# Kernel optimization log

Hardware: AMD Instinct MI355X
Metric: run time of the kernel (lower is better)

## Reference

```python
import jax, jax.numpy as jnp
import numpy as np

B, H, S, D = 4, 16, 2048, 64
SCALE = 8.0  # sqrt(D)
NEG = -1000000000.0


def setup_inputs() -> dict:
    key = jax.random.key(0)
    kq, kk, kv = jax.random.split(key, 3)
    q = jax.random.normal(kq, (B, H, S, D), dtype=jnp.float32)
    k = jax.random.normal(kk, (B, H, S, D), dtype=jnp.float32)
    v = jax.random.normal(kv, (B, H, S, D), dtype=jnp.float32)
    # causal mask: True means masked out (matches torch masked_fill)
    mask = jnp.triu(jnp.ones((S, S), dtype=bool), k=1)[None, None, :, :]
    mask = jnp.broadcast_to(mask, (B, 1, S, S))
    return {"q": q, "k": k, "v": v, "mask": mask}


def reference(q, k, v, mask):
    # score = q @ k^T / scale  -> [B,H,S,S]
    score = jnp.einsum("bhqd,bhkd->bhqk", q, k) / SCALE
    score = jnp.where(mask, NEG, score)
    probs = jax.nn.softmax(score, axis=-1)
    context = jnp.einsum("bhqk,bhkd->bhqd", probs, v)
    return context
```

## Files before the change

kernel.cpp:

```cpp
#include <hip/hip_runtime.h>

#define SQ 2048
#define DH 64
#define BK 64
#define NQT 32
#define NBH 64
#define M0 8.0f

#define WS_BYTES ((size_t)2 * NBH * SQ * DH * 2)

typedef float f32x4 __attribute__((ext_vector_type(4)));
typedef __bf16 bf16x8 __attribute__((ext_vector_type(8)));
typedef _Float16 f16x4 __attribute__((ext_vector_type(4)));
typedef __fp16 fp16x2 __attribute__((ext_vector_type(2)));
typedef unsigned short u16x8 __attribute__((ext_vector_type(8)));
typedef unsigned int u32x4 __attribute__((ext_vector_type(4)));

static __device__ __forceinline__ unsigned int pkbf(float a, float b) {
#if __has_builtin(__builtin_amdgcn_cvt_pk_bf16_f32)
  typedef __bf16 bf16x2 __attribute__((ext_vector_type(2)));
  bf16x2 r = __builtin_amdgcn_cvt_pk_bf16_f32(a, b);
  return __builtin_bit_cast(unsigned int, r);
#else
  unsigned int ua = __builtin_bit_cast(unsigned int, a);
  unsigned int ub = __builtin_bit_cast(unsigned int, b);
  ua += 0x7fffu + ((ua >> 16) & 1u);
  ub += 0x7fffu + ((ub >> 16) & 1u);
  return (ua >> 16) | (ub & 0xffff0000u);
#endif
}

static __device__ __forceinline__ unsigned int pkf16(float a, float b) {
  fp16x2 r = __builtin_amdgcn_cvt_pkrtz(a, b);
  return __builtin_bit_cast(unsigned int, r);
}

static __device__ __forceinline__ f32x4 mfma_qk(u16x8 a, u16x8 b, f32x4 c) {
  return __builtin_amdgcn_mfma_f32_16x16x32_bf16(
      __builtin_bit_cast(bf16x8, a), __builtin_bit_cast(bf16x8, b), c, 0, 0, 0);
}

static __device__ __forceinline__ f32x4 mfma_pv(f16x4 a, f16x4 b, f32x4 c) {
  return __builtin_amdgcn_mfma_f32_16x16x16f16(a, b, c, 0, 0, 0);
}

static __device__ __forceinline__ void ld16(unsigned short* l, const unsigned short* g) {
  __builtin_amdgcn_global_load_lds(
      (const __attribute__((address_space(1))) unsigned int*)(const void*)g,
      (__attribute__((address_space(3))) unsigned int*)(void*)l, 16, 0, 0);
}

static __device__ __forceinline__ void store_tile(float* wb, float* dst,
                                                  const f32x4* o, int lane,
                                                  int l15, int quad) {
#pragma unroll
  for (int dt = 0; dt < 4; ++dt) {
    const int colw = dt * 16 + quad * 4;
    *(f32x4*)&wb[l15 * 64 + (colw ^ ((l15 & 3) * 16))] = o[dt];
  }
  __builtin_amdgcn_wave_barrier();
#pragma unroll
  for (int j = 0; j < 4; ++j) {
    const int row = j * 4 + (lane >> 4);
    const int colw = (lane & 15) * 4;
    f32x4 v = *(const f32x4*)&wb[row * 64 + (colw ^ ((row & 3) * 16))];
    *(f32x4*)&dst[row * 64 + colw] = v;
  }
}

__global__ __launch_bounds__(256) void prep(const float* __restrict__ K,
                                            const float* __restrict__ V,
                                            unsigned short* __restrict__ Kb,
                                            unsigned short* __restrict__ Vt) {
  const int bh = (int)blockIdx.x >> 5;
  const int st = (int)blockIdx.x & 31;
  const int tid = threadIdx.x;
  __shared__ __align__(16) unsigned short T[DH * 64];
  {
    const int r = tid >> 2, c0 = (tid & 3) * 16;
    const float* kp = K + ((size_t)bh * SQ + st * 64 + r) * DH + c0;
    f32x4 x0 = *(const f32x4*)kp, x1 = *(const f32x4*)(kp + 4),
          x2 = *(const f32x4*)(kp + 8), x3 = *(const f32x4*)(kp + 12);
    u32x4 w0 = {pkbf(x0[0], x0[1]), pkbf(x0[2], x0[3]), pkbf(x1[0], x1[1]), pkbf(x1[2], x1[3])};
    u32x4 w1 = {pkbf(x2[0], x2[1]), pkbf(x2[2], x2[3]), pkbf(x3[0], x3[1]), pkbf(x3[2], x3[3])};
    unsigned short* kb = Kb + ((size_t)bh * SQ + st * 64 + r) * DH + c0;
    *(u32x4*)kb = w0;
    *(u32x4*)(kb + 8) = w1;
  }
  {
    const int kvb = (tid >> 4) * 4, vdb = (tid & 15) * 4;
    const float* vp = V + ((size_t)bh * SQ + st * 64 + kvb) * DH + vdb;
    f32x4 r0 = *(const f32x4*)vp, r1 = *(const f32x4*)(vp + DH),
          r2 = *(const f32x4*)(vp + 2 * DH), r3 = *(const f32x4*)(vp + 3 * DH);
    const int uu = kvb >> 3, h = (kvb >> 2) & 1;
#pragma unroll
    for (int i = 0; i < 4; ++i) {
      const int d = vdb + i;
      uint2 w = {pkf16(r0[i], r1[i]), pkf16(r2[i], r3[i])};
      *(uint2*)&T[d * 64 + ((uu ^ (d & 7)) * 8) + h * 4] = w;
    }
  }
  __syncthreads();
  {
    const int d2 = tid >> 2, cp = (tid & 3) * 2;
#pragma unroll
    for (int e = 0; e < 2; ++e) {
      const int uu = cp + e;
      u16x8 val = *(const u16x8*)&T[d2 * 64 + ((uu ^ (d2 & 7)) * 8)];
      *(u16x8*)&Vt[(size_t)bh * DH * SQ + (size_t)d2 * SQ + st * 64 + uu * 8] = val;
    }
  }
}

__global__ __launch_bounds__(256, 4) void fa_main(
    const float* __restrict__ Q, const unsigned short* __restrict__ Kb,
    const unsigned short* __restrict__ Vt, float* __restrict__ O) {
  const int lin = (int)blockIdx.x;
  const int xcd = lin & 7, u = lin >> 3, hh = u & 7, p = u >> 3;
  const int bh = hh * 8 + xcd;
  const int qtl = p, qth = NQT - 1 - p;

  const int tid = threadIdx.x;
  const int wv = tid >> 6;
  const int lane = tid & 63;
  const int l15 = lane & 15;
  const int quad = lane >> 4;

  __shared__ __align__(16) unsigned short S0[2 * BK * DH];
  __shared__ __align__(16) unsigned short S1[2 * BK * DH];

  const size_t hq = (size_t)bh * (SQ * DH);
  const unsigned short* KbH = Kb + (size_t)bh * SQ * DH;
  const unsigned short* VtH = Vt + (size_t)bh * DH * SQ;

  const int srow = wv * 16 + (lane >> 3);
  const int sc = lane & 7;

  u16x8 qfl[2], qfh[2];
  {
    const float scq = 0.125f * 1.4426950408889634f;
#pragma unroll
    for (int g = 0; g < 2; ++g) {
      const int wq0 = (g ? qth : qtl) * 64 + wv * 16;
      const float* qp = Q + hq + (size_t)(wq0 + l15) * DH + quad * 8;
#pragma unroll
      for (int c = 0; c < 2; ++c) {
        f32x4 x = *(const f32x4*)(qp + c * 32);
        f32x4 y = *(const f32x4*)(qp + c * 32 + 4);
        u32x4 w = {pkbf(x[0] * scq, x[1] * scq), pkbf(x[2] * scq, x[3] * scq),
                   pkbf(y[0] * scq, y[1] * scq), pkbf(y[2] * scq, y[3] * scq)};
        (g ? qfh : qfl)[c] = __builtin_bit_cast(u16x8, w);
      }
    }
  }

  f32x4 ol[4], oh[4], lal, lah;
#pragma unroll
  for (int dt = 0; dt < 4; ++dt) {
    ol[dt] = (f32x4){0.f, 0.f, 0.f, 0.f};
    oh[dt] = (f32x4){0.f, 0.f, 0.f, 0.f};
  }
  lal = (f32x4){0.f, 0.f, 0.f, 0.f};
  lah = (f32x4){0.f, 0.f, 0.f, 0.f};
  const f16x4 ones = {(_Float16)1.f, (_Float16)1.f, (_Float16)1.f, (_Float16)1.f};

  auto stage = [&](unsigned short* W, int t) {
    const int kb = t * BK;
    unsigned short* Kd = W;
    unsigned short* Vd = W + BK * DH;
#pragma unroll
    for (int j = 0; j < 2; ++j) {
      const int row = srow + j * 8;
      ld16(&Kd[row * 64 + sc * 8], &KbH[(size_t)(kb + row) * 64 + ((sc ^ (row & 7)) * 8)]);
      ld16(&Vd[row * 64 + sc * 8], &VtH[(size_t)row * SQ + kb + ((sc ^ (row & 7)) * 8)]);
    }
  };

  auto attend = [&](const unsigned short* R, const u16x8* qf, f32x4* o,
                    f32x4& la, bool diag) {
    const unsigned short* Ks = R;
    const unsigned short* Vs = R + BK * DH;
    f32x4 s[4];
#pragma unroll
    for (int nt = 0; nt < 4; ++nt) {
      f32x4 acc = {-M0, -M0, -M0, -M0};
#pragma unroll
      for (int c = 0; c < 2; ++c) {
        const int row = nt * 16 + l15;
        const int un = c * 4 + quad;
        u16x8 kf = *(const u16x8*)&Ks[row * 64 + ((un ^ (row & 7)) * 8)];
        acc = mfma_qk(kf, qf[c], acc);
      }
      s[nt] = acc;
    }
    if (diag) {
#pragma unroll
      for (int nt = 0; nt < 4; ++nt)
#pragma unroll
        for (int r = 0; r < 4; ++r)
          if (nt * 16 + quad * 4 + r > wv * 16 + l15) s[nt][r] = -1e30f;
    }
    f16x4 pf[4];
#pragma unroll
    for (int nt = 0; nt < 4; ++nt) {
      f32x4 pr;
#pragma unroll
      for (int r = 0; r < 4; ++r) pr[r] = __builtin_amdgcn_exp2f(s[nt][r]);
      uint2 w2 = {pkf16(pr[0], pr[1]), pkf16(pr[2], pr[3])};
      pf[nt] = __builtin_bit_cast(f16x4, w2);
    }
#pragma unroll
    for (int nt = 0; nt < 4; ++nt) la = mfma_pv(ones, pf[nt], la);
#pragma unroll
    for (int dt = 0; dt < 4; ++dt) {
      const int d = dt * 16 + l15;
#pragma unroll
      for (int nt = 0; nt < 4; ++nt) {
        const int uv = nt * 2 + (quad >> 1);
        f16x4 vf = *(const f16x4*)&Vs[d * 64 + ((uv ^ (d & 7)) * 8) + (quad & 1) * 4];
        o[dt] = mfma_pv(vf, pf[nt], o[dt]);
      }
    }
  };

  auto step = [&](int t, const unsigned short* R, unsigned short* W) {
    if (t <= qtl) attend(R, qfl, ol, lal, t == qtl);
    attend(R, qfh, oh, lah, t == qth);
    __syncthreads();
    if (t + 2 <= qth) stage(W, t + 2);
  };

  stage(S0, 0);
  __syncthreads();
  stage(S1, 1);
  for (int t = 0; t <= qth; t += 2) {
    step(t, S0, S0);
    if (t + 1 <= qth) step(t + 1, S1, S1);
  }

  float* wb = (float*)S0 + wv * 1024;
  {
    const float inv = 1.0f / lal[0];
    f32x4 on[4];
#pragma unroll
    for (int dt = 0; dt < 4; ++dt) on[dt] = ol[dt] * inv;
    store_tile(wb, O + hq + (size_t)(qtl * 64 + wv * 16) * DH, on, lane, l15, quad);
  }
  {
    const float inv = 1.0f / lah[0];
    f32x4 on[4];
#pragma unroll
    for (int dt = 0; dt < 4; ++dt) on[dt] = oh[dt] * inv;
    store_tile(wb, O + hq + (size_t)(qth * 64 + wv * 16) * DH, on, lane, l15, quad);
  }
}

__global__ __launch_bounds__(256, 4) void fa_full(
    const float* __restrict__ Q, const float* __restrict__ K,
    const float* __restrict__ V, float* __restrict__ O) {
  const int lin = (int)blockIdx.x;
  const int xcd = lin & 7;
  const int u = lin >> 3;
  const int hh = u & 7;
  const int p = u >> 3;
  const int bh = hh * 8 + xcd;
  const int tid = threadIdx.x;
  const int wv = tid >> 6;
  const int lane = tid & 63;
  const int l15 = lane & 15;
  const int quad = lane >> 4;
  __shared__ __align__(16) unsigned short SMEM[2][2 * BK * DH];
  const size_t hbase = (size_t)bh * (SQ * DH);
  const int krr = tid >> 3, kcc = (tid & 7) * 8;
  const int kvb = (tid >> 4) * 4, vdb = (tid & 15) * 4;
#pragma unroll
  for (int ph = 0; ph < 2; ++ph) {
    const int qt = ph ? (NQT - 1 - p) : p;
    const int wq0 = qt * 64 + wv * 16;
    u16x8 qf[2];
    {
      const float scq = 0.125f * 1.4426950408889634f;
      const float* qp = Q + hbase + (size_t)(wq0 + l15) * DH + quad * 8;
#pragma unroll
      for (int c = 0; c < 2; ++c) {
        f32x4 x = *(const f32x4*)(qp + c * 32);
        f32x4 y = *(const f32x4*)(qp + c * 32 + 4);
        u32x4 w = {pkbf(x[0] * scq, x[1] * scq), pkbf(x[2] * scq, x[3] * scq),
                   pkbf(y[0] * scq, y[1] * scq), pkbf(y[2] * scq, y[3] * scq)};
        qf[c] = __builtin_bit_cast(u16x8, w);
      }
    }
    f32x4 o[4];
#pragma unroll
    for (int dt = 0; dt < 4; ++dt) o[dt] = (f32x4){0.f, 0.f, 0.f, 0.f};
    float l = 0.f;
    f32x4 ka[2][2], va[4];
    {
      const float* kp = K + hbase + (size_t)krr * DH + kcc;
      ka[0][0] = *(const f32x4*)kp;             ka[0][1] = *(const f32x4*)(kp + 4);
      ka[1][0] = *(const f32x4*)(kp + 32 * DH); ka[1][1] = *(const f32x4*)(kp + 32 * DH + 4);
      const float* vp = V + hbase + (size_t)kvb * DH + vdb;
      va[0] = *(const f32x4*)vp;            va[1] = *(const f32x4*)(vp + DH);
      va[2] = *(const f32x4*)(vp + 2 * DH); va[3] = *(const f32x4*)(vp + 3 * DH);
    }
    __syncthreads();
    {
      unsigned short* Ksn = SMEM[0];
      unsigned short* Vsn = SMEM[0] + BK * DH;
#pragma unroll
      for (int h = 0; h < 2; ++h) {
        const int rr = h * 32 + krr;
        u32x4 w = {pkbf(ka[h][0][0], ka[h][0][1]), pkbf(ka[h][0][2], ka[h][0][3]),
                   pkbf(ka[h][1][0], ka[h][1][1]), pkbf(ka[h][1][2], ka[h][1][3])};
        *(u32x4*)&Ksn[rr * DH + (kcc ^ ((rr & 7) * 8))] = w;
      }
#pragma unroll
      for (int i = 0; i < 4; ++i) {
        const int d = vdb + i;
        uint2 w = {pkf16(va[0][i], va[1][i]), pkf16(va[2][i], va[3][i])};
        *(uint2*)&Vsn[d * BK + (kvb ^ ((d & 15) * 4))] = w;
      }
    }
    __syncthreads();
    for (int t = 0; t <= qt; ++t) {
      const unsigned short* Ks = SMEM[t & 1];
      const unsigned short* Vs = SMEM[t & 1] + BK * DH;
      if (t < qt) {
        const int kb2 = (t + 1) * BK;
        const float* kp = K + hbase + (size_t)(kb2 + krr) * DH + kcc;
        ka[0][0] = *(const f32x4*)kp;             ka[0][1] = *(const f32x4*)(kp + 4);
        ka[1][0] = *(const f32x4*)(kp + 32 * DH); ka[1][1] = *(const f32x4*)(kp + 32 * DH + 4);
        const float* vp = V + hbase + (size_t)(kb2 + kvb) * DH + vdb;
        va[0] = *(const f32x4*)vp;            va[1] = *(const f32x4*)(vp + DH);
        va[2] = *(const f32x4*)(vp + 2 * DH); va[3] = *(const f32x4*)(vp + 3 * DH);
      }
      f32x4 s[4];
#pragma unroll
      for (int nt = 0; nt < 4; ++nt) {
        f32x4 acc = {-M0, -M0, -M0, -M0};
#pragma unroll
        for (int c = 0; c < 2; ++c) {
          const int row = nt * 16 + l15;
          u16x8 kf = *(const u16x8*)&Ks[row * DH + ((c * 32 + quad * 8) ^ ((l15 & 7) * 8))];
          acc = mfma_qk(kf, qf[c], acc);
        }
        s[nt] = acc;
      }
      if (t == qt) {
#pragma unroll
        for (int nt = 0; nt < 4; ++nt)
#pragma unroll
          for (int r = 0; r < 4; ++r)
            if (nt * 16 + quad * 4 + r > wv * 16 + l15) s[nt][r] = -1e30f;
      }
      f16x4 pf[4];
#pragma unroll
      for (int nt = 0; nt < 4; ++nt) {
        f32x4 pr;
#pragma unroll
        for (int r = 0; r < 4; ++r) { pr[r] = __builtin_amdgcn_exp2f(s[nt][r]); l += pr[r]; }
        uint2 w2 = {pkf16(pr[0], pr[1]), pkf16(pr[2], pr[3])};
        pf[nt] = __builtin_bit_cast(f16x4, w2);
      }
#pragma unroll
      for (int dt = 0; dt < 4; ++dt) {
        const int d = dt * 16 + l15;
#pragma unroll
        for (int nt = 0; nt < 4; ++nt) {
          f16x4 vf = *(const f16x4*)&Vs[d * BK + ((nt * 16 + quad * 4) ^ (l15 * 4))];
          o[dt] = mfma_pv(vf, pf[nt], o[dt]);
        }
      }
      if (t < qt) {
        unsigned short* Ksn = SMEM[(t + 1) & 1];
        unsigned short* Vsn = SMEM[(t + 1) & 1] + BK * DH;
#pragma unroll
        for (int h = 0; h < 2; ++h) {
          const int rr = h * 32 + krr;
          u32x4 w = {pkbf(ka[h][0][0], ka[h][0][1]), pkbf(ka[h][0][2], ka[h][0][3]),
                     pkbf(ka[h][1][0], ka[h][1][1]), pkbf(ka[h][1][2], ka[h][1][3])};
          *(u32x4*)&Ksn[rr * DH + (kcc ^ ((rr & 7) * 8))] = w;
        }
#pragma unroll
        for (int i = 0; i < 4; ++i) {
          const int d = vdb + i;
          uint2 w = {pkf16(va[0][i], va[1][i]), pkf16(va[2][i], va[3][i])};
          *(uint2*)&Vsn[d * BK + (kvb ^ ((d & 15) * 4))] = w;
        }
        __syncthreads();
      }
    }
    l += __shfl_xor(l, 16, 64);
    l += __shfl_xor(l, 32, 64);
    const float inv = 1.0f / l;
    f32x4 on[4];
#pragma unroll
    for (int dt = 0; dt < 4; ++dt) on[dt] = o[dt] * inv;
    float* wb = (float*)SMEM[(qt + 1) & 1] + wv * 1024;
    store_tile(wb, O + hbase + (size_t)wq0 * DH, on, lane, l15, quad);
  }
}

extern "C" void kernel_launch(void* const* d_in, const int* in_sizes, int n_in,
                              void* d_out, int out_size, void* d_ws, size_t ws_size,
                              hipStream_t stream) {
  const float* q = (const float*)d_in[0];
  const float* k = (const float*)d_in[1];
  const float* v = (const float*)d_in[2];
  float* o = (float*)d_out;
  if (ws_size >= WS_BYTES) {
    unsigned short* Kb = (unsigned short*)d_ws;
    unsigned short* Vt = Kb + (size_t)NBH * SQ * DH;
    prep<<<dim3(NBH * 32), 256, 0, stream>>>(k, v, Kb, Vt);
    fa_main<<<dim3(1024), 256, 0, stream>>>(q, Kb, Vt, o);
  } else {
    fa_full<<<dim3(1024), 256, 0, stream>>>(q, k, v, o);
  }
}
```

Before: 217.8 us.

## Give each block one contiguous 128-row query tile with two 16-row fragments per wave

The main kernel stops pairing a low and a high 64-row query tile per block. Each block now owns one contiguous 128-row query tile, with each wave covering 32 rows as two fragments that share every K and V fragment loaded from LDS. Blocks are issued heaviest-first by reversing the tile index. This cuts LDS reads per MFMA and front-loads long blocks, but per-block work is no longer balanced, and half the waves idle during the final diagonal tile steps.

Result: faster. 209.7 us (-3.7%).

```diff
diff --git a/kernel.cpp b/kernel.cpp
--- a/kernel.cpp
+++ b/kernel.cpp
@@ -116,9 +116,11 @@
     const float* __restrict__ Q, const unsigned short* __restrict__ Kb,
     const unsigned short* __restrict__ Vt, float* __restrict__ O) {
   const int lin = (int)blockIdx.x;
-  const int xcd = lin & 7, u = lin >> 3, hh = u & 7, p = u >> 3;
+  const int xcd = lin & 7, u = lin >> 3;
+  const int hh = u & 7;
+  const int pi = 15 - (u >> 3);
   const int bh = hh * 8 + xcd;
-  const int qtl = p, qth = NQT - 1 - p;
+  const int tend = 2 * pi + 1;
 
   const int tid = threadIdx.x;
   const int wv = tid >> 6;
@@ -136,32 +138,35 @@
   const int srow = wv * 16 + (lane >> 3);
   const int sc = lane & 7;
 
-  u16x8 qfl[2], qfh[2];
+  const int qbase = pi * 128 + wv * 32;
+  const int dtw = 2 * pi + (wv >> 1);
+  const int qo = (wv & 1) * 32;
+
+  u16x8 qf[2][2];
   {
     const float scq = 0.125f * 1.4426950408889634f;
 #pragma unroll
-    for (int g = 0; g < 2; ++g) {
-      const int wq0 = (g ? qth : qtl) * 64 + wv * 16;
-      const float* qp = Q + hq + (size_t)(wq0 + l15) * DH + quad * 8;
+    for (int f = 0; f < 2; ++f) {
+      const float* qp = Q + hq + (size_t)(qbase + 16 * f + l15) * DH + quad * 8;
 #pragma unroll
       for (int c = 0; c < 2; ++c) {
         f32x4 x = *(const f32x4*)(qp + c * 32);
         f32x4 y = *(const f32x4*)(qp + c * 32 + 4);
         u32x4 w = {pkbf(x[0] * scq, x[1] * scq), pkbf(x[2] * scq, x[3] * scq),
                    pkbf(y[0] * scq, y[1] * scq), pkbf(y[2] * scq, y[3] * scq)};
-        (g ? qfh : qfl)[c] = __builtin_bit_cast(u16x8, w);
-      }
-    }
-  }
-
-  f32x4 ol[4], oh[4], lal, lah;
+        qf[f][c] = __builtin_bit_cast(u16x8, w);
+      }
+    }
+  }
+
+  f32x4 o0[4], o1[4], la0, la1;
 #pragma unroll
   for (int dt = 0; dt < 4; ++dt) {
-    ol[dt] = (f32x4){0.f, 0.f, 0.f, 0.f};
-    oh[dt] = (f32x4){0.f, 0.f, 0.f, 0.f};
-  }
-  lal = (f32x4){0.f, 0.f, 0.f, 0.f};
-  lah = (f32x4){0.f, 0.f, 0.f, 0.f};
+    o0[dt] = (f32x4){0.f, 0.f, 0.f, 0.f};
+    o1[dt] = (f32x4){0.f, 0.f, 0.f, 0.f};
+  }
+  la0 = (f32x4){0.f, 0.f, 0.f, 0.f};
+  la1 = (f32x4){0.f, 0.f, 0.f, 0.f};
   const f16x4 ones = {(_Float16)1.f, (_Float16)1.f, (_Float16)1.f, (_Float16)1.f};
 
   auto stage = [&](unsigned short* W, int t) {
@@ -176,41 +181,53 @@
     }
   };
 
-  auto attend = [&](const unsigned short* R, const u16x8* qf, f32x4* o,
-                    f32x4& la, bool diag) {
+  auto attend = [&](const unsigned short* R, bool diag) {
     const unsigned short* Ks = R;
     const unsigned short* Vs = R + BK * DH;
-    f32x4 s[4];
+    f32x4 s0[4], s1[4];
 #pragma unroll
     for (int nt = 0; nt < 4; ++nt) {
-      f32x4 acc = {-M0, -M0, -M0, -M0};
+      f32x4 a0 = {-M0, -M0, -M0, -M0}, a1 = {-M0, -M0, -M0, -M0};
 #pragma unroll
       for (int c = 0; c < 2; ++c) {
         const int row = nt * 16 + l15;
         const int un = c * 4 + quad;
         u16x8 kf = *(const u16x8*)&Ks[row * 64 + ((un ^ (row & 7)) * 8)];
-        acc = mfma_qk(kf, qf[c], acc);
-      }
-      s[nt] = acc;
+        a0 = mfma_qk(kf, qf[0][c], a0);
+        a1 = mfma_qk(kf, qf[1][c], a1);
+      }
+      s0[nt] = a0;
+      s1[nt] = a1;
     }
     if (diag) {
 #pragma unroll
       for (int nt = 0; nt < 4; ++nt)
 #pragma unroll
-        for (int r = 0; r < 4; ++r)
-          if (nt * 16 + quad * 4 + r > wv * 16 + l15) s[nt][r] = -1e30f;
-    }
-    f16x4 pf[4];
+        for (int r = 0; r < 4; ++r) {
+          const int kvl = nt * 16 + quad * 4 + r;
+          if (kvl > qo + l15) s0[nt][r] = -1e30f;
+          if (kvl > qo + 16 + l15) s1[nt][r] = -1e30f;
+        }
+    }
+    f16x4 pf0[4], pf1[4];
 #pragma unroll
     for (int nt = 0; nt < 4; ++nt) {
-      f32x4 pr;
-#pragma unroll
-      for (int r = 0; r < 4; ++r) pr[r] = __builtin_amdgcn_exp2f(s[nt][r]);
-      uint2 w2 = {pkf16(pr[0], pr[1]), pkf16(pr[2], pr[3])};
-      pf[nt] = __builtin_bit_cast(f16x4, w2);
-    }
-#pragma unroll
-    for (int nt = 0; nt < 4; ++nt) la = mfma_pv(ones, pf[nt], la);
+      f32x4 p0, p1;
+#pragma unroll
+      for (int r = 0; r < 4; ++r) {
+        p0[r] = __builtin_amdgcn_exp2f(s0[nt][r]);
+        p1[r] = __builtin_amdgcn_exp2f(s1[nt][r]);
+      }
+      uint2 w0 = {pkf16(p0[0], p0[1]), pkf16(p0[2], p0[3])};
+      uint2 w1 = {pkf16(p1[0], p1[1]), pkf16(p1[2], p1[3])};
+      pf0[nt] = __builtin_bit_cast(f16x4, w0);
+      pf1[nt] = __builtin_bit_cast(f16x4, w1);
+    }
+#pragma unroll
+    for (int nt = 0; nt < 4; ++nt) {
+      la0 = mfma_pv(ones, pf0[nt], la0);
+      la1 = mfma_pv(ones, pf1[nt], la1);
+    }
 #pragma unroll
     for (int dt = 0; dt < 4; ++dt) {
       const int d = dt * 16 + l15;
@@ -218,40 +235,40 @@
       for (int nt = 0; nt < 4; ++nt) {
         const int uv = nt * 2 + (quad >> 1);
         f16x4 vf = *(const f16x4*)&Vs[d * 64 + ((uv ^ (d & 7)) * 8) + (quad & 1) * 4];
-        o[dt] = mfma_pv(vf, pf[nt], o[dt]);
+        o0[dt] = mfma_pv(vf, pf0[nt], o0[dt]);
+        o1[dt] = mfma_pv(vf, pf1[nt], o1[dt]);
       }
     }
   };
 
   auto step = [&](int t, const unsigned short* R, unsigned short* W) {
-    if (t <= qtl) attend(R, qfl, ol, lal, t == qtl);
-    attend(R, qfh, oh, lah, t == qth);
+    if (t <= dtw) attend(R, t == dtw);
     __syncthreads();
-    if (t + 2 <= qth) stage(W, t + 2);
+    if (t + 2 <= tend) stage(W, t + 2);
   };
 
   stage(S0, 0);
   __syncthreads();
   stage(S1, 1);
-  for (int t = 0; t <= qth; t += 2) {
+  for (int t = 0; t <= tend; t += 2) {
     step(t, S0, S0);
-    if (t + 1 <= qth) step(t + 1, S1, S1);
+    if (t + 1 <= tend) step(t + 1, S1, S1);
   }
 
   float* wb = (float*)S0 + wv * 1024;
   {
-    const float inv = 1.0f / lal[0];
+    const float inv = 1.0f / la0[0];
     f32x4 on[4];
 #pragma unroll
-    for (int dt = 0; dt < 4; ++dt) on[dt] = ol[dt] * inv;
-    store_tile(wb, O + hq + (size_t)(qtl * 64 + wv * 16) * DH, on, lane, l15, quad);
-  }
-  {
-    const float inv = 1.0f / lah[0];
+    for (int dt = 0; dt < 4; ++dt) on[dt] = o0[dt] * inv;
+    store_tile(wb, O + hq + (size_t)(qbase)*DH, on, lane, l15, quad);
+  }
+  {
+    const float inv = 1.0f / la1[0];
     f32x4 on[4];
 #pragma unroll
-    for (int dt = 0; dt < 4; ++dt) on[dt] = oh[dt] * inv;
-    store_tile(wb, O + hq + (size_t)(qth * 64 + wv * 16) * DH, on, lane, l15, quad);
+    for (int dt = 0; dt < 4; ++dt) on[dt] = o1[dt] * inv;
+    store_tile(wb, O + hq + (size_t)(qbase + 16) * DH, on, lane, l15, quad);
   }
 }
 
```
